# Optimization experiments

Measured on AMD Instinct MI355X. Metric: run time of the kernel, lower is better.

Reference implementation:

```python
import jax, jax.numpy as jnp
import numpy as np

D_MODEL = 1024
NUM_HEADS = 16
D_K = D_MODEL // NUM_HEADS


def setup_inputs() -> dict:
    key = jax.random.key(0)
    ks = jax.random.split(key, 11)
    B, S = 4, 2048
    s = 1.0 / np.sqrt(D_MODEL)
    return {
        "Q": jax.random.normal(ks[0], (B, S, D_MODEL), jnp.float32),
        "K": jax.random.normal(ks[1], (B, S, D_MODEL), jnp.float32),
        "V": jax.random.normal(ks[2], (B, S, D_MODEL), jnp.float32),
        "Wq": jax.random.normal(ks[3], (D_MODEL, D_MODEL), jnp.float32) * s,
        "bq": jax.random.normal(ks[4], (D_MODEL,), jnp.float32) * 0.01,
        "Wk": jax.random.normal(ks[5], (D_MODEL, D_MODEL), jnp.float32) * s,
        "bk": jax.random.normal(ks[6], (D_MODEL,), jnp.float32) * 0.01,
        "Wv": jax.random.normal(ks[7], (D_MODEL, D_MODEL), jnp.float32) * s,
        "bv": jax.random.normal(ks[8], (D_MODEL,), jnp.float32) * 0.01,
        "Wo": jax.random.normal(ks[9], (D_MODEL, D_MODEL), jnp.float32) * s,
        "bo": jax.random.normal(ks[10], (D_MODEL,), jnp.float32) * 0.01,
    }


def _split_heads(x):
    B, S, _ = x.shape
    return x.reshape(B, S, NUM_HEADS, D_K).transpose(0, 2, 1, 3)  # [B,H,S,Dk]


def reference(Q, K, V, Wq, bq, Wk, bk, Wv, bv, Wo, bo):
    # Linear layers (torch nn.Linear: x @ W.T + b)
    q = _split_heads(Q @ Wq.T + bq)
    k = _split_heads(K @ Wk.T + bk)
    v = _split_heads(V @ Wv.T + bv)
    scale = 1.0 / jnp.sqrt(jnp.asarray(D_K, jnp.float32))
    scores = jnp.einsum('bhqd,bhkd->bhqk', q, k) * scale  # [B,H,S,S]
    attn = jax.nn.softmax(scores, axis=-1)
    ctx = jnp.einsum('bhqk,bhkd->bhqd', attn, v)  # [B,H,S,Dk]
    B, H, S, Dk = ctx.shape
    ctx = ctx.transpose(0, 2, 1, 3).reshape(B, S, H * Dk)
    return ctx @ Wo.T + bo
```

## Files before the change

### kernel.cpp

```cpp
#include <hip/hip_runtime.h>
#include <hip/hip_bf16.h>

#define B_SZ 4
#define S_SZ 2048
#define D_SZ 1024
#define H_SZ 16
#define DK_SZ 64
#define M_ROWS (B_SZ * S_SZ)

typedef __bf16 bf16x8 __attribute__((ext_vector_type(8)));
typedef __bf16 bf16x4 __attribute__((ext_vector_type(4)));
typedef float  f32x4  __attribute__((ext_vector_type(4)));

typedef __attribute__((address_space(3))) unsigned int lds_u32;
typedef const __attribute__((address_space(1))) unsigned int glob_u32;

__device__ __forceinline__ bf16x8 load8(const float* p) {
    f32x4 a = *(const f32x4*)p;
    f32x4 b = *(const f32x4*)(p + 4);
    bf16x8 r;
    r[0] = (__bf16)a[0]; r[1] = (__bf16)a[1]; r[2] = (__bf16)a[2]; r[3] = (__bf16)a[3];
    r[4] = (__bf16)b[0]; r[5] = (__bf16)b[1]; r[6] = (__bf16)b[2]; r[7] = (__bf16)b[3];
    return r;
}
__device__ __forceinline__ bf16x8 load8(const __bf16* p) {
    return *(const bf16x8*)p;
}

__global__ __launch_bounds__(256)
void conv_bf16(const float* __restrict__ in, __bf16* __restrict__ out, int n8) {
    int i = blockIdx.x * 256 + threadIdx.x;
    const int stride = gridDim.x * 256;
    for (; i < n8; i += stride)
        *(bf16x8*)&out[(size_t)i * 8] = load8(in + (size_t)i * 8);
}

#define SAST 72
template <typename TA, typename TW, typename TC>
__global__ __launch_bounds__(256, 2)
void gemm_nt_bias(const TA* __restrict__ A, const TW* __restrict__ W,
                  const float* __restrict__ bias, TC* __restrict__ C,
                  int M, int N, int K) {
    __shared__ __align__(16) __bf16 sA[128 * SAST];
    __shared__ __align__(16) __bf16 sB[128 * SAST];
    const int tid = threadIdx.x;
    const int w = tid >> 6, lane = tid & 63;
    const int m0 = blockIdx.x * 128, n0 = blockIdx.y * 128;
    const int wr = w >> 1, wc = w & 1;
    const int lr = lane & 15, lq = lane >> 4;

    f32x4 acc[4][4] = {};

    for (int kt = 0; kt < K; kt += 64) {
        for (int it = 0; it < 4; ++it) {
            const int c = it * 256 + tid;
            const int row = c >> 3, col8 = c & 7;
            *(bf16x8*)&sA[row * SAST + col8 * 8] =
                load8(A + (size_t)(m0 + row) * K + kt + col8 * 8);
            *(bf16x8*)&sB[row * SAST + col8 * 8] =
                load8(W + (size_t)(n0 + row) * K + kt + col8 * 8);
        }
        __syncthreads();
        for (int s = 0; s < 2; ++s) {
            bf16x8 av[4], bv[4];
            for (int i = 0; i < 4; ++i)
                av[i] = *(const bf16x8*)&sA[(wr * 64 + i * 16 + lr) * SAST + s * 32 + lq * 8];
            for (int j = 0; j < 4; ++j)
                bv[j] = *(const bf16x8*)&sB[(wc * 64 + j * 16 + lr) * SAST + s * 32 + lq * 8];
            for (int i = 0; i < 4; ++i)
                for (int j = 0; j < 4; ++j)
                    acc[i][j] = __builtin_amdgcn_mfma_f32_16x16x32_bf16(
                        av[i], bv[j], acc[i][j], 0, 0, 0);
        }
        __syncthreads();
    }
    for (int j = 0; j < 4; ++j) {
        const int col = n0 + wc * 64 + j * 16 + lr;
        const float bias_f = bias[col];
        for (int i = 0; i < 4; ++i) {
            const int rbase = m0 + wr * 64 + i * 16 + lq * 4;
            for (int r = 0; r < 4; ++r)
                C[(size_t)(rbase + r) * N + col] = (TC)(acc[i][j][r] + bias_f);
        }
    }
}

#define KVB 64
#define PST 72
__global__ __launch_bounds__(256, 2)
void attn_kernel(const __bf16* qm, const __bf16* __restrict__ km,
                 const __bf16* __restrict__ vm, __bf16* ctx) {
    __shared__ __align__(16) __bf16 sK[KVB * 64];
    __shared__ __align__(16) __bf16 sVt[64 * KVB];
    __shared__ __align__(16) __bf16 sP[8][16 * PST];

    const int tid = threadIdx.x, w = tid >> 6, lane = tid & 63;
    const int lr = lane & 15, lq = lane >> 4;
    const int bh = blockIdx.y, b = bh >> 4, h = bh & 15;
    const int q0 = blockIdx.x * 128;
    const size_t rowbase = (size_t)b * S_SZ;
    const int hoff = h * DK_SZ;

    bf16x8 qf[2][2];
#pragma unroll
    for (int qs = 0; qs < 2; ++qs) {
        const __bf16* qp = qm + (rowbase + q0 + w * 32 + qs * 16 + lr) * D_SZ + hoff;
        qf[qs][0] = *(const bf16x8*)(qp + lq * 8);
        qf[qs][1] = *(const bf16x8*)(qp + 32 + lq * 8);
    }

    float mrow[2] = {-1e30f, -1e30f};
    float lrow[2] = {0.f, 0.f};
    f32x4 o[2][4] = {};

    const int gl_koff = (lane >> 3);
    const int gl_c8 = lane & 7;
    const int v_key7 = tid >> 3, v_d8 = tid & 7;

    const __bf16* kbase = km + rowbase * D_SZ + hoff;
    const __bf16* vbase = vm + rowbase * D_SZ + hoff;

    for (int k0 = 0; k0 < S_SZ; k0 += KVB) {
#pragma unroll
        for (int i = 0; i < 2; ++i) {
            const int key = w * 16 + i * 8 + gl_koff;
            const __bf16* gp = kbase + (size_t)(k0 + key) * D_SZ
                               + ((gl_c8 ^ gl_koff) << 3);
            __builtin_amdgcn_global_load_lds(
                (glob_u32*)gp, (lds_u32*)(&sK[(w * 2 + i) * 512]), 16, 0, 0);
        }
#pragma unroll
        for (int p = 0; p < 2; ++p) {
            const int key = p * 32 + v_key7;
            bf16x8 vv = *(const bf16x8*)(vbase + (size_t)(k0 + key) * D_SZ + (v_d8 << 3));
            const int colbase = (((key >> 3) ^ v_d8) << 3) + (key & 7);
#pragma unroll
            for (int e = 0; e < 8; ++e)
                sVt[(v_d8 * 8 + e) * 64 + colbase] = vv[e];
        }
        __syncthreads();

        f32x4 sc[2][4] = {};
#pragma unroll
        for (int s = 0; s < 2; ++s) {
            bf16x8 kf[4];
#pragma unroll
            for (int nt = 0; nt < 4; ++nt)
                kf[nt] = *(const bf16x8*)&sK[(nt * 16 + lr) * 64
                                             + (((s * 4 + lq) ^ (lr & 7)) << 3)];
#pragma unroll
            for (int nt = 0; nt < 4; ++nt) {
                sc[0][nt] = __builtin_amdgcn_mfma_f32_16x16x32_bf16(
                    kf[nt], qf[0][s], sc[0][nt], 0, 0, 0);
                sc[1][nt] = __builtin_amdgcn_mfma_f32_16x16x32_bf16(
                    kf[nt], qf[1][s], sc[1][nt], 0, 0, 0);
            }
        }

#pragma unroll
        for (int qs = 0; qs < 2; ++qs) {
            float sv[4][4];
            float mt = -1e30f;
#pragma unroll
            for (int nt = 0; nt < 4; ++nt)
#pragma unroll
                for (int r = 0; r < 4; ++r) {
                    sv[nt][r] = sc[qs][nt][r] * 0.125f;
                    mt = fmaxf(mt, sv[nt][r]);
                }
            mt = fmaxf(mt, __shfl_xor(mt, 16));
            mt = fmaxf(mt, __shfl_xor(mt, 32));
            if (!__all(mt - mrow[qs] <= 8.f)) {
                const float mn = fmaxf(mrow[qs], mt);
                const float al = __expf(mrow[qs] - mn);
                mrow[qs] = mn;
                lrow[qs] *= al;
                float a4[4];
#pragma unroll
                for (int r = 0; r < 4; ++r)
                    a4[r] = __shfl(al, ((lane >> 4) << 2) + r, 64);
#pragma unroll
                for (int nt = 0; nt < 4; ++nt)
#pragma unroll
                    for (int r = 0; r < 4; ++r)
                        o[qs][nt][r] *= a4[r];
            }
            float ls = 0.f;
#pragma unroll
            for (int nt = 0; nt < 4; ++nt) {
                bf16x4 pk;
#pragma unroll
                for (int r = 0; r < 4; ++r) {
                    const float pv = __expf(sv[nt][r] - mrow[qs]);
                    ls += pv;
                    pk[r] = (__bf16)pv;
                }
                *(bf16x4*)&sP[w * 2 + qs][lr * PST + nt * 16 + lq * 4] = pk;
            }
            ls += __shfl_xor(ls, 16);
            ls += __shfl_xor(ls, 32);
            lrow[qs] += ls;
        }

        bf16x8 pf[2][2];
#pragma unroll
        for (int qs = 0; qs < 2; ++qs)
#pragma unroll
            for (int s = 0; s < 2; ++s)
                pf[qs][s] = *(const bf16x8*)&sP[w * 2 + qs][lr * PST + s * 32 + lq * 8];
#pragma unroll
        for (int s = 0; s < 2; ++s)
#pragma unroll
            for (int nt = 0; nt < 4; ++nt) {
                bf16x8 vf = *(const bf16x8*)&sVt[
                    (nt * 16 + lr) * 64
                    + (((s * 4 + lq) ^ (nt * 2 + (lr >> 3))) << 3)];
                o[0][nt] = __builtin_amdgcn_mfma_f32_16x16x32_bf16(
                    pf[0][s], vf, o[0][nt], 0, 0, 0);
                o[1][nt] = __builtin_amdgcn_mfma_f32_16x16x32_bf16(
                    pf[1][s], vf, o[1][nt], 0, 0, 0);
            }
        __syncthreads();
    }

#pragma unroll
    for (int qs = 0; qs < 2; ++qs) {
        const float linv = 1.f / lrow[qs];
        float l4[4];
#pragma unroll
        for (int r = 0; r < 4; ++r)
            l4[r] = __shfl(linv, ((lane >> 4) << 2) + r, 64);
#pragma unroll
        for (int nt = 0; nt < 4; ++nt) {
            const int col = hoff + nt * 16 + lr;
#pragma unroll
            for (int r = 0; r < 4; ++r) {
                const size_t row = rowbase + q0 + w * 32 + qs * 16 + lq * 4 + r;
                ctx[row * D_SZ + col] = (__bf16)(o[qs][nt][r] * l4[r]);
            }
        }
    }
}

extern "C" void kernel_launch(void* const* d_in, const int* in_sizes, int n_in,
                              void* d_out, int out_size, void* d_ws, size_t ws_size,
                              hipStream_t stream) {
    const float* Q  = (const float*)d_in[0];
    const float* K  = (const float*)d_in[1];
    const float* V  = (const float*)d_in[2];
    const float* Wq = (const float*)d_in[3];
    const float* bq = (const float*)d_in[4];
    const float* Wk = (const float*)d_in[5];
    const float* bk = (const float*)d_in[6];
    const float* Wv = (const float*)d_in[7];
    const float* bv = (const float*)d_in[8];
    const float* Wo = (const float*)d_in[9];
    const float* bo = (const float*)d_in[10];
    float* out = (float*)d_out;

    const size_t plane = (size_t)M_ROWS * D_SZ;
    const size_t wsz   = (size_t)D_SZ * D_SZ;
    const dim3 gg(M_ROWS / 128, D_SZ / 128), bb(256);
    const dim3 ag(S_SZ / 128, B_SZ * H_SZ);

    const size_t need_fast = (3 * plane + 4 * wsz) * sizeof(__bf16);
    if (ws_size >= need_fast) {
        __bf16* s0  = (__bf16*)d_ws;
        __bf16* qw  = s0 + plane;
        __bf16* kw  = s0 + 2 * plane;
        __bf16* wgt = s0 + 3 * plane;
        __bf16* vw  = (__bf16*)d_out;
        const int p8 = (int)(plane / 8), w8 = (int)(wsz / 8);

        conv_bf16<<<512, bb, 0, stream>>>(Wq, wgt, w8);
        conv_bf16<<<512, bb, 0, stream>>>(Wk, wgt + wsz, w8);
        conv_bf16<<<512, bb, 0, stream>>>(Wv, wgt + 2 * wsz, w8);
        conv_bf16<<<512, bb, 0, stream>>>(Wo, wgt + 3 * wsz, w8);

        conv_bf16<<<2048, bb, 0, stream>>>(Q, s0, p8);
        gemm_nt_bias<__bf16, __bf16, __bf16><<<gg, bb, 0, stream>>>(
            s0, wgt, bq, qw, M_ROWS, D_SZ, D_SZ);
        conv_bf16<<<2048, bb, 0, stream>>>(K, s0, p8);
        gemm_nt_bias<__bf16, __bf16, __bf16><<<gg, bb, 0, stream>>>(
            s0, wgt + wsz, bk, kw, M_ROWS, D_SZ, D_SZ);
        conv_bf16<<<2048, bb, 0, stream>>>(V, s0, p8);
        gemm_nt_bias<__bf16, __bf16, __bf16><<<gg, bb, 0, stream>>>(
            s0, wgt + 2 * wsz, bv, vw, M_ROWS, D_SZ, D_SZ);

        attn_kernel<<<ag, bb, 0, stream>>>(qw, kw, vw, qw);

        gemm_nt_bias<__bf16, __bf16, float><<<gg, bb, 0, stream>>>(
            qw, wgt + 3 * wsz, bo, out, M_ROWS, D_SZ, D_SZ);
        return;
    }

    if (ws_size < 2 * plane * sizeof(__bf16)) return;
    __bf16* qw = (__bf16*)d_ws;
    __bf16* kw = qw + plane;
    __bf16* vw = (__bf16*)d_out;
    __bf16* cw = qw;

    gemm_nt_bias<float, float, __bf16><<<gg, bb, 0, stream>>>(Q, Wq, bq, qw, M_ROWS, D_SZ, D_SZ);
    gemm_nt_bias<float, float, __bf16><<<gg, bb, 0, stream>>>(K, Wk, bk, kw, M_ROWS, D_SZ, D_SZ);
    gemm_nt_bias<float, float, __bf16><<<gg, bb, 0, stream>>>(V, Wv, bv, vw, M_ROWS, D_SZ, D_SZ);

    attn_kernel<<<ag, bb, 0, stream>>>(qw, kw, vw, cw);

    gemm_nt_bias<__bf16, float, float><<<gg, bb, 0, stream>>>(cw, Wo, bo, out,
                                                              M_ROWS, D_SZ, D_SZ);
}
```

Measured before the change: 424.0 us.

## Add direct global-to-LDS GEMM kernel with XOR-swizzled shared layout

Adds a new bf16 GEMM variant that stages tiles with global_load_lds, copying straight from global memory into LDS without passing through registers. The LDS layout is unpadded and XOR-swizzled by row to avoid bank conflicts. The four projection GEMMs on the fast path use this kernel, with the aim of cutting register pressure and load-instruction overhead in the main loop. It is still single-buffered, so loads do not overlap compute across k-tiles, and its correctness depends on the swizzle matching the per-lane layout of the direct LDS loads.

```diff
diff --git a/kernel.cpp b/kernel.cpp
--- a/kernel.cpp
+++ b/kernel.cpp
@@ -33,6 +33,71 @@
     const int stride = gridDim.x * 256;
     for (; i < n8; i += stride)
         *(bf16x8*)&out[(size_t)i * 8] = load8(in + (size_t)i * 8);
+}
+
+template <typename TC>
+__global__ __launch_bounds__(256, 2)
+void gemm_nt_bias_g(const __bf16* __restrict__ A, const __bf16* __restrict__ W,
+                    const float* __restrict__ bias, TC* __restrict__ C,
+                    int M, int N, int K) {
+    __shared__ __align__(16) __bf16 sA[128 * 64];
+    __shared__ __align__(16) __bf16 sB[128 * 64];
+    const int tid = threadIdx.x;
+    const int w = tid >> 6, lane = tid & 63;
+    const int m0 = blockIdx.x * 128, n0 = blockIdx.y * 128;
+    const int wr = w >> 1, wc = w & 1;
+    const int lr = lane & 15, lq = lane >> 4;
+
+    const int st_roff = lane >> 3;
+    const int st_cg   = (lane & 7) ^ st_roff;
+
+    f32x4 acc[4][4] = {};
+
+    for (int kt = 0; kt < K; kt += 64) {
+#pragma unroll
+        for (int i = 0; i < 4; ++i) {
+            const int seg = i * 4 + w;
+            const int row = seg * 8 + st_roff;
+            __builtin_amdgcn_global_load_lds(
+                (glob_u32*)(A + (size_t)(m0 + row) * K + kt + st_cg * 8),
+                (lds_u32*)(&sA[seg * 512]), 16, 0, 0);
+            __builtin_amdgcn_global_load_lds(
+                (glob_u32*)(W + (size_t)(n0 + row) * K + kt + st_cg * 8),
+                (lds_u32*)(&sB[seg * 512]), 16, 0, 0);
+        }
+        __syncthreads();
+#pragma unroll
+        for (int s = 0; s < 2; ++s) {
+            bf16x8 av[4], bv[4];
+#pragma unroll
+            for (int i = 0; i < 4; ++i)
+                av[i] = *(const bf16x8*)&sA[(wr * 64 + i * 16 + lr) * 64
+                                            + (((s * 4 + lq) ^ (lr & 7)) << 3)];
+#pragma unroll
+            for (int j = 0; j < 4; ++j)
+                bv[j] = *(const bf16x8*)&sB[(wc * 64 + j * 16 + lr) * 64
+                                            + (((s * 4 + lq) ^ (lr & 7)) << 3)];
+#pragma unroll
+            for (int i = 0; i < 4; ++i)
+#pragma unroll
+                for (int j = 0; j < 4; ++j)
+                    acc[i][j] = __builtin_amdgcn_mfma_f32_16x16x32_bf16(
+                        av[i], bv[j], acc[i][j], 0, 0, 0);
+        }
+        __syncthreads();
+    }
+#pragma unroll
+    for (int j = 0; j < 4; ++j) {
+        const int col = n0 + wc * 64 + j * 16 + lr;
+        const float bias_f = bias[col];
+#pragma unroll
+        for (int i = 0; i < 4; ++i) {
+            const int rbase = m0 + wr * 64 + i * 16 + lq * 4;
+#pragma unroll
+            for (int r = 0; r < 4; ++r)
+                C[(size_t)(rbase + r) * N + col] = (TC)(acc[i][j][r] + bias_f);
+        }
+    }
 }
 
 #define SAST 72
@@ -278,18 +343,18 @@
         conv_bf16<<<512, bb, 0, stream>>>(Wo, wgt + 3 * wsz, w8);
 
         conv_bf16<<<2048, bb, 0, stream>>>(Q, s0, p8);
-        gemm_nt_bias<__bf16, __bf16, __bf16><<<gg, bb, 0, stream>>>(
+        gemm_nt_bias_g<__bf16><<<gg, bb, 0, stream>>>(
             s0, wgt, bq, qw, M_ROWS, D_SZ, D_SZ);
         conv_bf16<<<2048, bb, 0, stream>>>(K, s0, p8);
-        gemm_nt_bias<__bf16, __bf16, __bf16><<<gg, bb, 0, stream>>>(
+        gemm_nt_bias_g<__bf16><<<gg, bb, 0, stream>>>(
             s0, wgt + wsz, bk, kw, M_ROWS, D_SZ, D_SZ);
         conv_bf16<<<2048, bb, 0, stream>>>(V, s0, p8);
-        gemm_nt_bias<__bf16, __bf16, __bf16><<<gg, bb, 0, stream>>>(
+        gemm_nt_bias_g<__bf16><<<gg, bb, 0, stream>>>(
             s0, wgt + 2 * wsz, bv, vw, M_ROWS, D_SZ, D_SZ);
 
         attn_kernel<<<ag, bb, 0, stream>>>(qw, kw, vw, qw);
 
-        gemm_nt_bias<__bf16, __bf16, float><<<gg, bb, 0, stream>>>(
+        gemm_nt_bias_g<float><<<gg, bb, 0, stream>>>(
             qw, wgt + 3 * wsz, bo, out, M_ROWS, D_SZ, D_SZ);
         return;
     }
```

Result: faster. 395.2 us (-6.8%).
